# Optimization experiments

Measured on AMD Instinct MI355X. Metric: run time of the kernel, lower is better.

## Reference

```python
import jax, jax.numpy as jnp
import numpy as np

# ---- static geometry derived from truncation (matches torch __init__) ----
T = 127
N_LAT_NH = T + 1                                   # 128 NH latitudes
LONS = [20 + 4 * i for i in range(N_LAT_NH)]       # octahedral reduced grid
CUMS = np.concatenate([[0], np.cumsum(np.array(LONS + LONS[::-1]))]).astype(int)
HZW_NH = np.minimum(4 + np.arange(N_LAT_NH), T)    # cubic truncation: m_max = nlon//4 - 1, capped at T
N_LATS_PER_M = np.array([(HZW_NH >= m).sum() for m in range(T + 1)])
L_SYM_FULL = (T + 3) // 2                          # 65 rows before dropping row 0
L_ANT = (T + 2) // 2                               # 64
N_VARS = 128
BATCH, ENS = 4, 1


def _tri_masks():
    """Zero-padded triangular structure of the per-m Legendre matrices."""
    sym = np.zeros((T + 1, L_SYM_FULL, N_LAT_NH), np.float32)
    ant = np.zeros((T + 1, L_ANT, N_LAT_NH), np.float32)
    for m in range(T + 1):
        n_lats = int(N_LATS_PER_M[m])
        ms = (T - m + 3) // 2
        off = L_SYM_FULL - ms
        sym[m, off:, N_LAT_NH - n_lats:] = 1.0
        if (m + 1) % 2 == 1:
            sym[m, off, :] = 0.0
        ma = (T - m + 2) // 2
        off = L_ANT - ma
        ant[m, off:, N_LAT_NH - n_lats:] = 1.0
        if m % 2 == 1:
            ant[m, off, :] = 0.0
    return sym[:, 1:, :], ant   # module drops first symmetric row -> [128,64,128]


def setup_inputs() -> dict:
    key = jax.random.key(0)
    k1, k2, k3 = jax.random.split(key, 3)
    n_grid = int(CUMS[-1])
    x = jax.random.normal(k1, (BATCH, ENS, n_grid, N_VARS), jnp.float32)
    sm, am = _tri_masks()
    # random stand-ins for (gaussian-weight-fused) Legendre polynomials, with the exact
    # triangular zero structure the module builds from ecTrans assets
    symmetric = jax.random.normal(k2, sm.shape, jnp.float32) * jnp.asarray(sm)
    antisymmetric = jax.random.normal(k3, am.shape, jnp.float32) * jnp.asarray(am)
    return {"x": x, "symmetric": symmetric, "antisymmetric": antisymmetric}


def reference(x, symmetric, antisymmetric):
    """Octahedral SHT forward: ragged longitudinal rfft -> hemispheric fold -> per-m Legendre matmuls.

    Returns spectrum [b, e, l, m, vars, 2] (real/imag stacked on last axis).
    """
    n_lat = 2 * N_LAT_NH
    north, south = [], []
    # loop is over structurally distinct (ragged) latitude ring lengths; NH lat i and its
    # SH mirror (lat n_lat-1-i) share nlon/truncation, so batch them in one FFT call.
    for i in range(N_LAT_NH):
        j = n_lat - 1 - i
        nlon = LONS[i]
        xn = x[:, :, CUMS[i]:CUMS[i + 1], :]           # [b,e,nlon,v]
        xs = x[:, :, CUMS[j]:CUMS[j + 1], :]
        xp = jnp.stack([xn, xs], axis=2)               # [b,e,2,nlon,v]
        f = jnp.fft.rfft(xp, axis=3) / nlon            # torch norm='forward'
        m_hi = int(HZW_NH[i]) + 1                      # keep m <= highest zonal wavenumber
        f = f[:, :, :, :m_hi, :]
        f = jnp.pad(f, ((0, 0), (0, 0), (0, 0), (0, T + 1 - m_hi), (0, 0)))
        north.append(f[:, :, 0])
        south.append(f[:, :, 1])                       # index i <-> lat n_lat-1-i: already pole-mirrored
    north = jnp.stack(north, axis=2)                   # [b,e,n_lat_nh,m,v] complex64
    south = jnp.stack(south, axis=2)
    # hemispheric symmetry of Legendre polynomials
    sym = north + south
    anti = north - south
    # per-m truncated Legendre contractions over NH latitudes (n)
    out_s = jnp.einsum('mln,benmv->belmv', symmetric, sym)     # [b,e,64,m,v]
    out_a = jnp.einsum('mln,benmv->belmv', antisymmetric, anti)
    # interleave symmetric (l-m even) and antisymmetric (l-m odd) rows -> full l axis (128)
    spec = jnp.stack([out_s, out_a], axis=3)
    b, e, L, _, M, V = spec.shape
    spec = spec.reshape(b, e, 2 * L, M, V)             # [b,e,l,m,v] complex, lower triangle zeros
    return jnp.stack([spec.real, spec.imag], axis=-1)  # real view [b,e,l,m,v,2]
```

## Files before the change

### kernel.cpp

```cpp
#include <hip/hip_runtime.h>
#include <hip/hip_bf16.h>

#define NGRID 70144
#define NV 128

typedef float f32x4 __attribute__((ext_vector_type(4)));
typedef short short8 __attribute__((ext_vector_type(8)));

__device__ __forceinline__ unsigned f2bf(float f){
  return (unsigned)__bfloat16_as_ushort(__float2bfloat16(f));
}
__device__ __forceinline__ float bf2f(unsigned h){ return __uint_as_float(h<<16); }
__device__ __forceinline__ unsigned packsplit(float f){
  unsigned h = f2bf(f);
  unsigned l = f2bf(f - bf2f(h));
  return (h<<16) | l;
}
__device__ __forceinline__ int swzc(int c){ return (c ^ (c>>3)) & 7; }

__device__ __forceinline__ void unpack_frag(int4 a, int4 b, short8 &bh, short8 &bl){
  int h0 = (int)(((unsigned)a.x >> 16) | ((unsigned)a.y & 0xFFFF0000u));
  int h1 = (int)(((unsigned)a.z >> 16) | ((unsigned)a.w & 0xFFFF0000u));
  int h2 = (int)(((unsigned)b.x >> 16) | ((unsigned)b.y & 0xFFFF0000u));
  int h3 = (int)(((unsigned)b.z >> 16) | ((unsigned)b.w & 0xFFFF0000u));
  int l0 = (int)(((unsigned)a.x & 0xFFFFu) | ((unsigned)a.y << 16));
  int l1 = (int)(((unsigned)a.z & 0xFFFFu) | ((unsigned)a.w << 16));
  int l2 = (int)(((unsigned)b.x & 0xFFFFu) | ((unsigned)b.y << 16));
  int l3 = (int)(((unsigned)b.z & 0xFFFFu) | ((unsigned)b.w << 16));
  int4 H = make_int4(h0,h1,h2,h3), L = make_int4(l0,l1,l2,l3);
  bh = *(short8*)&H; bl = *(short8*)&L;
}

struct TileT { unsigned char ring, type, vh; };
constexpr int NTILES = 512;
struct Tiles { TileT t[NTILES]; };
constexpr Tiles make_tiles(){
  Tiles T{}; int k=0;
  for(int g=0; g<16; g++){
    for(int var=0; var<4; var++)
      for(int q=0; q<8; q++){
        int r = 127-(g*8+q);
        T.t[k].ring=(unsigned char)r;
        T.t[k].type=(unsigned char)(var>>1);
        T.t[k].vh  =(unsigned char)(var&1);
        k++;
      }
  }
  return T;
}
__constant__ Tiles TILES = make_tiles();

struct Offs { long o[129]; };
constexpr Offs make_offs(){
  Offs O{}; long off=0;
  for(int r=0;r<128;r++){
    O.o[r]=off;
    int mh=(5+r<128)?(5+r):128, jc=11+2*r;
    off += 4L*(((mh+15)/16)*16)*(((jc+31)/32)*32);
  }
  O.o[128]=off;
  return O;
}
__constant__ Offs TWOFF = make_offs();
constexpr long TWATOT = make_offs().o[128];

__global__ void fill_tw(unsigned short* __restrict__ twA){
  int ring = blockIdx.x, t = blockIdx.y, mq = blockIdx.z;
  int N = 20+4*ring, H = N/2, JC = H+1;
  int mhi = (5+ring<128)?(5+ring):128;
  int Mpad = ((mhi+15)>>4)<<4;
  int Kpad = ((JC+31)>>5)<<5;
  long MK = (long)Mpad*Kpad;
  unsigned short* hiT = twA + TWOFF.o[ring] + (long)(t*2)*MK;
  unsigned short* loT = hiT + MK;
  float invN = 1.0f/(float)N;
  int tid = threadIdx.x;
  for(int m=mq; m<Mpad; m+=4){
    int p0   = (int)(((long)m*tid) % N);
    int step = (int)(((long)m*256) % N);
    int p = p0;
    for(int j=tid;j<Kpad;j+=256){
      float val = 0.f;
      if(m < mhi && j < JC){
        float th = 6.2831853071795864f * (float)p * invN;
        float sn, cs; __sincosf(th,&sn,&cs);
        val = (t ? -sn : cs) * invN;
      }
      unsigned h = f2bf(val);
      unsigned l = f2bf(val - bf2f(h));
      long idx = (long)m*Kpad + j;
      hiT[idx] = (unsigned short)h;
      loT[idx] = (unsigned short)l;
      p += step; if(p>=N) p-=N;
    }
  }
}

__global__ __launch_bounds__(256,3) void dft_mfma(const float* __restrict__ x,
                                                  const unsigned short* __restrict__ twA,
                                                  unsigned* __restrict__ Gp){
  TileT tl = TILES.t[blockIdx.x];
  int ring = tl.ring, type = tl.type, vh = tl.vh;
  int b = blockIdx.y;
  int N = 20+4*ring, H = N/2, JC = H+1;
  int mhi = (5+ring<128)?(5+ring):128;
  int MtN = (mhi+15)>>4;
  int KT = (JC+31)>>5;
  int Kpad = KT<<5;
  int Mpad = MtN<<4;

  long MK = (long)Mpad*Kpad;
  const unsigned short* Ahi = twA + TWOFF.o[ring] + (long)(type*2)*MK;
  const unsigned short* Alo = Ahi + MK;

  const float* xn = x + ((long)b*NGRID + (long)ring*(2*ring+18))*NV;
  long a1 = ring+1;
  const float* xs = x + ((long)b*NGRID + (NGRID - a1*(2*a1+18)))*NV;

  __shared__ __align__(16) unsigned Bp[4096];

  int tid = threadIdx.x;
  int jb = tid >> 5;
  int vp = tid & 31;
  int vo = vh*64 + vp*2;
  int wave = tid >> 6, lane = tid & 63;
  int jj = lane & 15, kb = lane >> 4;

  f32x4 acc[8][2];
  #pragma unroll
  for(int Mt=0;Mt<8;Mt++){ acc[Mt][0]=(f32x4){0.f,0.f,0.f,0.f}; acc[Mt][1]=(f32x4){0.f,0.f,0.f,0.f}; }

  float2 rn[4], rs[4], rpn[4], rps[4];
  #define LOADX(KT_)                                              \
  {                                                               \
    int ktl = (KT_);                                              \
    _Pragma("unroll")                                             \
    for(int dj=0;dj<4;dj++){                                      \
      int j = ktl*32 + jb*4 + dj;                                 \
      float2 zz = make_float2(0.f,0.f);                           \
      rn[dj]=zz; rs[dj]=zz; rpn[dj]=zz; rps[dj]=zz;               \
      if(j < JC){                                                 \
        rn[dj] = *(const float2*)&xn[(long)j*NV + vo];            \
        rs[dj] = *(const float2*)&xs[(long)j*NV + vo];            \
        if(j > 0 && j < H){                                       \
          int jp = N - j;                                         \
          rpn[dj] = *(const float2*)&xn[(long)jp*NV + vo];        \
          rps[dj] = *(const float2*)&xs[(long)jp*NV + vo];        \
        }                                                         \
      }                                                           \
    }                                                             \
  }

  LOADX(0);
  for(int kt=0; kt<KT; ++kt){
    int4 w0, w1, w2, w3;
    {
      float sx[4], sy[4], ax[4], ay[4];
      #pragma unroll
      for(int dj=0;dj<4;dj++){
        float ex=rn[dj].x+rs[dj].x, ey=rn[dj].y+rs[dj].y;
        float ox=rn[dj].x-rs[dj].x, oy=rn[dj].y-rs[dj].y;
        float epx=rpn[dj].x+rps[dj].x, epy=rpn[dj].y+rps[dj].y;
        float opx=rpn[dj].x-rps[dj].x, opy=rpn[dj].y-rps[dj].y;
        sx[dj] = type ? (ex-epx) : (ex+epx);
        sy[dj] = type ? (ey-epy) : (ey+epy);
        ax[dj] = type ? (ox-opx) : (ox+opx);
        ay[dj] = type ? (oy-opy) : (oy+opy);
      }
      w0 = make_int4((int)packsplit(sx[0]),(int)packsplit(sx[1]),
                     (int)packsplit(sx[2]),(int)packsplit(sx[3]));
      w1 = make_int4((int)packsplit(ax[0]),(int)packsplit(ax[1]),
                     (int)packsplit(ax[2]),(int)packsplit(ax[3]));
      w2 = make_int4((int)packsplit(sy[0]),(int)packsplit(sy[1]),
                     (int)packsplit(sy[2]),(int)packsplit(sy[3]));
      w3 = make_int4((int)packsplit(ay[0]),(int)packsplit(ay[1]),
                     (int)packsplit(ay[2]),(int)packsplit(ay[3]));
    }
    __syncthreads();
    {
      int c0 = vp*4;
      *(int4*)&Bp[(c0+0)*32 + ((jb*4) ^ (swzc(c0+0)<<2))] = w0;
      *(int4*)&Bp[(c0+1)*32 + ((jb*4) ^ (swzc(c0+1)<<2))] = w1;
      *(int4*)&Bp[(c0+2)*32 + ((jb*4) ^ (swzc(c0+2)<<2))] = w2;
      *(int4*)&Bp[(c0+3)*32 + ((jb*4) ^ (swzc(c0+3)<<2))] = w3;
    }
    __syncthreads();
    if(kt+1 < KT) LOADX(kt+1);
    short8 bh[2], bl[2];
    #pragma unroll
    for(int ct=0;ct<2;ct++){
      int c = wave*32 + ct*16 + jj;
      int sw = swzc(c)<<2;
      int4 pa = *(const int4*)&Bp[c*32 + ((kb*8) ^ sw)];
      int4 pb = *(const int4*)&Bp[c*32 + ((kb*8+4) ^ sw)];
      unpack_frag(pa, pb, bh[ct], bl[ct]);
    }
    #pragma unroll
    for(int Mt=0;Mt<8;Mt++){
      if(Mt < MtN){
        long ao = (long)(Mt*16 + jj)*Kpad + kt*32 + kb*8;
        short8 ah = *(const short8*)&Ahi[ao];
        short8 al = *(const short8*)&Alo[ao];
        #pragma unroll
        for(int ct=0;ct<2;ct++){
          acc[Mt][ct] = __builtin_amdgcn_mfma_f32_16x16x32_bf16(ah, bh[ct], acc[Mt][ct], 0,0,0);
          acc[Mt][ct] = __builtin_amdgcn_mfma_f32_16x16x32_bf16(al, bh[ct], acc[Mt][ct], 0,0,0);
          acc[Mt][ct] = __builtin_amdgcn_mfma_f32_16x16x32_bf16(ah, bl[ct], acc[Mt][ct], 0,0,0);
        }
      }
    }
  }
  #pragma unroll
  for(int Mt=0;Mt<8;Mt++){
    if(Mt < MtN){
      #pragma unroll
      for(int ct=0;ct<2;ct++){
        int cg = vh*128 + wave*32 + ct*16 + jj;
        int s = cg & 1, v = cg >> 1;
        #pragma unroll
        for(int reg=0;reg<4;reg++){
          int m = Mt*16 + (kb<<2) + reg;
          if(m < mhi){
            Gp[(long)((s*2+type)*128 + m)*65536 + (long)ring*512 + b*128 + v]
              = packsplit(acc[Mt][ct][reg]);
          }
        }
      }
    }
  }
  #undef LOADX
}

__global__ void w_split(const float* __restrict__ Wsym, const float* __restrict__ Want,
                        unsigned short* __restrict__ Wh, unsigned short* __restrict__ Wl){
  long i = (long)blockIdx.x*256 + threadIdx.x;
  const float* W = (i < 1048576) ? Wsym : Want;
  float w = W[i & 1048575];
  unsigned h = f2bf(w);
  unsigned l = f2bf(w - bf2f(h));
  Wh[i] = (unsigned short)h;
  Wl[i] = (unsigned short)l;
}

__global__ __launch_bounds__(256) void legendre_mfma(const unsigned short* __restrict__ Wh,
                                                     const unsigned short* __restrict__ Wl,
                                                     const unsigned* __restrict__ Gp,
                                                     float* __restrict__ out){
  int m = blockIdx.x, b = blockIdx.y, s = blockIdx.z;
  __shared__ __align__(16) unsigned Bp[8192];
  int tid = threadIdx.x;
  int wave = tid >> 6, lane = tid & 63;
  int jj = lane & 15, kb = lane >> 4;

  int kt0 = (m > 4) ? ((m-4) >> 5) : 0;

  const unsigned short* WA = Wh + (long)(s*128+m)*8192;
  const unsigned short* WB = Wl + (long)(s*128+m)*8192;
  int ri = tid & 1, v = tid >> 1;
  long gC0 = (long)((s*2+ri)*128 + m)*65536 + (long)b*128 + v;

  f32x4 acc[4][4];
  #pragma unroll
  for(int a=0;a<4;a++)
    #pragma unroll
    for(int q=0;q<4;q++) acc[a][q] = (f32x4){0.f,0.f,0.f,0.f};

  int swT = swzc(tid)<<2;
  for(int kt=kt0; kt<4; ++kt){
    __syncthreads();
    #pragma unroll
    for(int k4=0;k4<32;k4+=4){
      int4 w = make_int4((int)Gp[gC0 + (long)(kt*32+k4+0)*512],
                         (int)Gp[gC0 + (long)(kt*32+k4+1)*512],
                         (int)Gp[gC0 + (long)(kt*32+k4+2)*512],
                         (int)Gp[gC0 + (long)(kt*32+k4+3)*512]);
      *(int4*)&Bp[tid*32 + (k4 ^ swT)] = w;
    }
    __syncthreads();
    short8 bh[4], bl[4];
    #pragma unroll
    for(int nt=0;nt<4;nt++){
      int c = (wave*4+nt)*16 + jj;
      int sw = swzc(c)<<2;
      int4 pa = *(const int4*)&Bp[c*32 + ((kb*8) ^ sw)];
      int4 pb = *(const int4*)&Bp[c*32 + ((kb*8+4) ^ sw)];
      unpack_frag(pa, pb, bh[nt], bl[nt]);
    }
    #pragma unroll
    for(int Mt=0;Mt<4;Mt++){
      long ao = (long)(Mt*16 + jj)*128 + kt*32 + kb*8;
      short8 ah = *(const short8*)&WA[ao];
      short8 al = *(const short8*)&WB[ao];
      #pragma unroll
      for(int nt=0;nt<4;nt++){
        acc[Mt][nt] = __builtin_amdgcn_mfma_f32_16x16x32_bf16(ah, bh[nt], acc[Mt][nt], 0,0,0);
        acc[Mt][nt] = __builtin_amdgcn_mfma_f32_16x16x32_bf16(al, bh[nt], acc[Mt][nt], 0,0,0);
        acc[Mt][nt] = __builtin_amdgcn_mfma_f32_16x16x32_bf16(ah, bl[nt], acc[Mt][nt], 0,0,0);
      }
    }
  }
  int r4 = (lane>>4)<<2;
  #pragma unroll
  for(int Mt=0;Mt<4;Mt++){
    #pragma unroll
    for(int nt=0;nt<4;nt++){
      int c = (wave*4+nt)*16 + jj;
      #pragma unroll
      for(int reg=0;reg<4;reg++){
        int l = Mt*16 + r4 + reg;
        out[((long)(b*128 + 2*l + s)*128 + m)*256 + c] = acc[Mt][nt][reg];
      }
    }
  }
}

extern "C" void kernel_launch(void* const* d_in, const int* in_sizes, int n_in,
                              void* d_out, int out_size, void* d_ws, size_t ws_size,
                              hipStream_t stream) {
  const float* x    = (const float*)d_in[0];
  const float* Wsym = (const float*)d_in[1];
  const float* Want = (const float*)d_in[2];
  float* out = (float*)d_out;

  size_t gpOffB = (size_t)TWATOT*2;
  if(gpOffB < 8388608) gpOffB = 8388608;
  gpOffB = (gpOffB + 255) & ~(size_t)255;

  unsigned short* twA = (unsigned short*)d_ws;
  unsigned* Gp = (unsigned*)((char*)d_ws + gpOffB);
  unsigned short* Wh = (unsigned short*)d_ws;
  unsigned short* Wl = Wh + 2097152;

  hipLaunchKernelGGL(fill_tw,       dim3(128,2,4),   dim3(256), 0, stream, twA);
  hipLaunchKernelGGL(dft_mfma,      dim3(NTILES,4),  dim3(256), 0, stream, x, twA, Gp);
  hipLaunchKernelGGL(w_split,       dim3(8192),      dim3(256), 0, stream, Wsym, Want, Wh, Wl);
  hipLaunchKernelGGL(legendre_mfma, dim3(128,4,2),   dim3(256), 0, stream, Wh, Wl, Gp, out);
}
```

Baseline: 357.7 us.

## Drop LDS staging; load MFMA B fragments directly from global with new Gp layout

Both the FFT-fold kernel and the Legendre kernel stop staging B operands through swizzled shared memory with block barriers. Each lane now gathers its fragment elements straight from global memory, and the intermediate Gp buffer is re-laid out so each column index is contiguous. The Legendre kernel also gets a launch-bounds occupancy hint. This removes LDS traffic and synchronisation, but replaces vectorised coalesced loads with many scalar strided global loads per lane and drops the software prefetch.

```diff
diff --git a/kernel.cpp b/kernel.cpp
--- a/kernel.cpp
+++ b/kernel.cpp
@@ -15,20 +15,6 @@
   unsigned h = f2bf(f);
   unsigned l = f2bf(f - bf2f(h));
   return (h<<16) | l;
-}
-__device__ __forceinline__ int swzc(int c){ return (c ^ (c>>3)) & 7; }
-
-__device__ __forceinline__ void unpack_frag(int4 a, int4 b, short8 &bh, short8 &bl){
-  int h0 = (int)(((unsigned)a.x >> 16) | ((unsigned)a.y & 0xFFFF0000u));
-  int h1 = (int)(((unsigned)a.z >> 16) | ((unsigned)a.w & 0xFFFF0000u));
-  int h2 = (int)(((unsigned)b.x >> 16) | ((unsigned)b.y & 0xFFFF0000u));
-  int h3 = (int)(((unsigned)b.z >> 16) | ((unsigned)b.w & 0xFFFF0000u));
-  int l0 = (int)(((unsigned)a.x & 0xFFFFu) | ((unsigned)a.y << 16));
-  int l1 = (int)(((unsigned)a.z & 0xFFFFu) | ((unsigned)a.w << 16));
-  int l2 = (int)(((unsigned)b.x & 0xFFFFu) | ((unsigned)b.y << 16));
-  int l3 = (int)(((unsigned)b.z & 0xFFFFu) | ((unsigned)b.w << 16));
-  int4 H = make_int4(h0,h1,h2,h3), L = make_int4(l0,l1,l2,l3);
-  bh = *(short8*)&H; bl = *(short8*)&L;
 }
 
 struct TileT { unsigned char ring, type, vh; };
@@ -117,83 +103,44 @@
   long a1 = ring+1;
   const float* xs = x + ((long)b*NGRID + (NGRID - a1*(2*a1+18)))*NV;
 
-  __shared__ __align__(16) unsigned Bp[4096];
-
-  int tid = threadIdx.x;
-  int jb = tid >> 5;
-  int vp = tid & 31;
-  int vo = vh*64 + vp*2;
-  int wave = tid >> 6, lane = tid & 63;
+  int lane = threadIdx.x & 63, wave = threadIdx.x >> 6;
   int jj = lane & 15, kb = lane >> 4;
 
+  int cg0 = vh*128 + wave*32 + jj;
+  int v0 = cg0 >> 1,        par0 = cg0 & 1;
+  int v1 = (cg0+16) >> 1,   par1 = (cg0+16) & 1;
+
   f32x4 acc[8][2];
   #pragma unroll
   for(int Mt=0;Mt<8;Mt++){ acc[Mt][0]=(f32x4){0.f,0.f,0.f,0.f}; acc[Mt][1]=(f32x4){0.f,0.f,0.f,0.f}; }
 
-  float2 rn[4], rs[4], rpn[4], rps[4];
-  #define LOADX(KT_)                                              \
-  {                                                               \
-    int ktl = (KT_);                                              \
-    _Pragma("unroll")                                             \
-    for(int dj=0;dj<4;dj++){                                      \
-      int j = ktl*32 + jb*4 + dj;                                 \
-      float2 zz = make_float2(0.f,0.f);                           \
-      rn[dj]=zz; rs[dj]=zz; rpn[dj]=zz; rps[dj]=zz;               \
-      if(j < JC){                                                 \
-        rn[dj] = *(const float2*)&xn[(long)j*NV + vo];            \
-        rs[dj] = *(const float2*)&xs[(long)j*NV + vo];            \
-        if(j > 0 && j < H){                                       \
-          int jp = N - j;                                         \
-          rpn[dj] = *(const float2*)&xn[(long)jp*NV + vo];        \
-          rps[dj] = *(const float2*)&xs[(long)jp*NV + vo];        \
-        }                                                         \
-      }                                                           \
-    }                                                             \
-  }
-
-  LOADX(0);
   for(int kt=0; kt<KT; ++kt){
-    int4 w0, w1, w2, w3;
-    {
-      float sx[4], sy[4], ax[4], ay[4];
-      #pragma unroll
-      for(int dj=0;dj<4;dj++){
-        float ex=rn[dj].x+rs[dj].x, ey=rn[dj].y+rs[dj].y;
-        float ox=rn[dj].x-rs[dj].x, oy=rn[dj].y-rs[dj].y;
-        float epx=rpn[dj].x+rps[dj].x, epy=rpn[dj].y+rps[dj].y;
-        float opx=rpn[dj].x-rps[dj].x, opy=rpn[dj].y-rps[dj].y;
-        sx[dj] = type ? (ex-epx) : (ex+epx);
-        sy[dj] = type ? (ey-epy) : (ey+epy);
-        ax[dj] = type ? (ox-opx) : (ox+opx);
-        ay[dj] = type ? (oy-opy) : (oy+opy);
-      }
-      w0 = make_int4((int)packsplit(sx[0]),(int)packsplit(sx[1]),
-                     (int)packsplit(sx[2]),(int)packsplit(sx[3]));
-      w1 = make_int4((int)packsplit(ax[0]),(int)packsplit(ax[1]),
-                     (int)packsplit(ax[2]),(int)packsplit(ax[3]));
-      w2 = make_int4((int)packsplit(sy[0]),(int)packsplit(sy[1]),
-                     (int)packsplit(sy[2]),(int)packsplit(sy[3]));
-      w3 = make_int4((int)packsplit(ay[0]),(int)packsplit(ay[1]),
-                     (int)packsplit(ay[2]),(int)packsplit(ay[3]));
-    }
-    __syncthreads();
-    {
-      int c0 = vp*4;
-      *(int4*)&Bp[(c0+0)*32 + ((jb*4) ^ (swzc(c0+0)<<2))] = w0;
-      *(int4*)&Bp[(c0+1)*32 + ((jb*4) ^ (swzc(c0+1)<<2))] = w1;
-      *(int4*)&Bp[(c0+2)*32 + ((jb*4) ^ (swzc(c0+2)<<2))] = w2;
-      *(int4*)&Bp[(c0+3)*32 + ((jb*4) ^ (swzc(c0+3)<<2))] = w3;
-    }
-    __syncthreads();
-    if(kt+1 < KT) LOADX(kt+1);
     short8 bh[2], bl[2];
     #pragma unroll
     for(int ct=0;ct<2;ct++){
-      int c = wave*32 + ct*16 + jj;
-      int sw = swzc(c)<<2;
-      int4 pa = *(const int4*)&Bp[c*32 + ((kb*8) ^ sw)];
-      int4 pb = *(const int4*)&Bp[c*32 + ((kb*8+4) ^ sw)];
-      unpack_frag(pa, pb, bh[ct], bl[ct]);
+      int v  = ct ? v1 : v0;
+      int par= ct ? par1 : par0;
+      #pragma unroll
+      for(int e=0;e<8;e++){
+        int j = kt*32 + kb*8 + e;
+        float vn=0.f, vs=0.f, vpn=0.f, vps=0.f;
+        if(j < JC){
+          vn = xn[(long)j*NV + v];
+          vs = xs[(long)j*NV + v];
+          if(j > 0 && j < H){
+            int jp = N - j;
+            vpn = xn[(long)jp*NV + v];
+            vps = xs[(long)jp*NV + v];
+          }
+        }
+        float base = par ? (vn - vs) : (vn + vs);
+        float mirr = par ? (vpn - vps) : (vpn + vps);
+        float val  = type ? (base - mirr) : (base + mirr);
+        unsigned h = f2bf(val);
+        unsigned lo = f2bf(val - bf2f(h));
+        bh[ct][e] = (short)h;
+        bl[ct][e] = (short)lo;
+      }
     }
     #pragma unroll
     for(int Mt=0;Mt<8;Mt++){
@@ -215,20 +162,19 @@
     if(Mt < MtN){
       #pragma unroll
       for(int ct=0;ct<2;ct++){
-        int cg = vh*128 + wave*32 + ct*16 + jj;
+        int cg = cg0 + ct*16;
         int s = cg & 1, v = cg >> 1;
         #pragma unroll
         for(int reg=0;reg<4;reg++){
           int m = Mt*16 + (kb<<2) + reg;
           if(m < mhi){
-            Gp[(long)((s*2+type)*128 + m)*65536 + (long)ring*512 + b*128 + v]
+            Gp[(((long)(s*128 + m)*128 + ring)*1024) + b*256 + v*2 + type]
               = packsplit(acc[Mt][ct][reg]);
           }
         }
       }
     }
   }
-  #undef LOADX
 }
 
 __global__ void w_split(const float* __restrict__ Wsym, const float* __restrict__ Want,
@@ -242,22 +188,19 @@
   Wl[i] = (unsigned short)l;
 }
 
-__global__ __launch_bounds__(256) void legendre_mfma(const unsigned short* __restrict__ Wh,
-                                                     const unsigned short* __restrict__ Wl,
-                                                     const unsigned* __restrict__ Gp,
-                                                     float* __restrict__ out){
+__global__ __launch_bounds__(256,3) void legendre_mfma(const unsigned short* __restrict__ Wh,
+                                                       const unsigned short* __restrict__ Wl,
+                                                       const unsigned* __restrict__ Gp,
+                                                       float* __restrict__ out){
   int m = blockIdx.x, b = blockIdx.y, s = blockIdx.z;
-  __shared__ __align__(16) unsigned Bp[8192];
-  int tid = threadIdx.x;
-  int wave = tid >> 6, lane = tid & 63;
+  int lane = threadIdx.x & 63, wave = threadIdx.x >> 6;
   int jj = lane & 15, kb = lane >> 4;
 
   int kt0 = (m > 4) ? ((m-4) >> 5) : 0;
 
   const unsigned short* WA = Wh + (long)(s*128+m)*8192;
   const unsigned short* WB = Wl + (long)(s*128+m)*8192;
-  int ri = tid & 1, v = tid >> 1;
-  long gC0 = (long)((s*2+ri)*128 + m)*65536 + (long)b*128 + v;
+  long gBase = ((long)(s*128 + m)*128)*1024 + b*256;
 
   f32x4 acc[4][4];
   #pragma unroll
@@ -265,26 +208,18 @@
     #pragma unroll
     for(int q=0;q<4;q++) acc[a][q] = (f32x4){0.f,0.f,0.f,0.f};
 
-  int swT = swzc(tid)<<2;
   for(int kt=kt0; kt<4; ++kt){
-    __syncthreads();
-    #pragma unroll
-    for(int k4=0;k4<32;k4+=4){
-      int4 w = make_int4((int)Gp[gC0 + (long)(kt*32+k4+0)*512],
-                         (int)Gp[gC0 + (long)(kt*32+k4+1)*512],
-                         (int)Gp[gC0 + (long)(kt*32+k4+2)*512],
-                         (int)Gp[gC0 + (long)(kt*32+k4+3)*512]);
-      *(int4*)&Bp[tid*32 + (k4 ^ swT)] = w;
-    }
-    __syncthreads();
     short8 bh[4], bl[4];
     #pragma unroll
     for(int nt=0;nt<4;nt++){
       int c = (wave*4+nt)*16 + jj;
-      int sw = swzc(c)<<2;
-      int4 pa = *(const int4*)&Bp[c*32 + ((kb*8) ^ sw)];
-      int4 pb = *(const int4*)&Bp[c*32 + ((kb*8+4) ^ sw)];
-      unpack_frag(pa, pb, bh[nt], bl[nt]);
+      #pragma unroll
+      for(int e=0;e<8;e++){
+        int n = kt*32 + kb*8 + e;
+        unsigned p = Gp[gBase + (long)n*1024 + c];
+        bh[nt][e] = (short)(p >> 16);
+        bl[nt][e] = (short)(p & 0xFFFFu);
+      }
     }
     #pragma unroll
     for(int Mt=0;Mt<4;Mt++){
```

New measurement: 388.4 us. 1.09x slower.
